# Performance work log

Hardware: AMD Instinct MI355X
Metric: run time of the kernel (lower is better)

Reference implementation:

```python
import jax, jax.numpy as jnp
import numpy as np

NUM_CENTERS = 256
CAPACITY = 2048
FEAT_DIM = 768
BATCH = 65536


def setup_inputs() -> dict:
    key = jax.random.key(0)
    k_bank, k_cid, k_idx = jax.random.split(key, 3)
    bank = jax.random.normal(k_bank, (NUM_CENTERS, CAPACITY, FEAT_DIM), dtype=jnp.float32)
    target_center_ids = jax.random.randint(k_cid, (BATCH,), 0, NUM_CENTERS, dtype=jnp.int64)
    rand_idx = jax.random.randint(k_idx, (BATCH,), 0, CAPACITY, dtype=jnp.int64)
    return {"bank": bank, "target_center_ids": target_center_ids, "rand_idx": rand_idx}


def reference(bank, target_center_ids, rand_idx):
    # get_counterfactual_noise(strategy='random') with a full bank:
    # per-sample gather bank[c_i, r_i] -> [B, feat_dim]
    return bank[target_center_ids, rand_idx]
```

## Files before the change

### kernel.cpp

```cpp
#include <hip/hip_runtime.h>

#define NUM_CENTERS 256
#define CAPACITY    2048
#define FEAT_DIM    768
#define BATCH       65536
#define VEC_PER_ROW (FEAT_DIM / 4)

#define THREADS 256
#define BLOCKS  2048

typedef float f32x4 __attribute__((ext_vector_type(4)));

__global__ __launch_bounds__(THREADS, 8) void gather_rows_kernel(
        const f32x4* __restrict__ bank,
        const int*   __restrict__ center_ids,
        const int*   __restrict__ rand_idx,
        f32x4*       __restrict__ out) {
    const int lane   = threadIdx.x & 63;
    const int wave   = (blockIdx.x << 2) | (threadIdx.x >> 6);
    const int nwaves = BLOCKS * (THREADS / 64);

#pragma unroll 2
    for (int s = wave; s < BATCH; s += nwaves) {
        const int c = __builtin_amdgcn_readfirstlane(center_ids[s]);
        const int r = __builtin_amdgcn_readfirstlane(rand_idx[s]);

        const f32x4* __restrict__ src =
            bank + ((long long)c * CAPACITY + (long long)r) * (long long)VEC_PER_ROW;
        f32x4* __restrict__ dst = out + (long long)s * (long long)VEC_PER_ROW;

        const f32x4 a = src[lane];
        const f32x4 b = src[lane + 64];
        const f32x4 d = src[lane + 128];
        __builtin_nontemporal_store(a, &dst[lane]);
        __builtin_nontemporal_store(b, &dst[lane + 64]);
        __builtin_nontemporal_store(d, &dst[lane + 128]);
    }
}

extern "C" void kernel_launch(void* const* d_in, const int* in_sizes, int n_in,
                              void* d_out, int out_size, void* d_ws, size_t ws_size,
                              hipStream_t stream) {
    const f32x4* bank       = (const f32x4*)d_in[0];
    const int*   center_ids = (const int*)d_in[1];
    const int*   rand_idx   = (const int*)d_in[2];
    f32x4*       out        = (f32x4*)d_out;

    gather_rows_kernel<<<BLOCKS, THREADS, 0, stream>>>(bank, center_ids, rand_idx, out);
}
```

Measured before the change: 1.816 ms.

## Launch one block per gathered row instead of grid-stride waves

```diff
diff --git a/kernel.cpp b/kernel.cpp
--- a/kernel.cpp
+++ b/kernel.cpp
@@ -6,36 +6,22 @@
 #define BATCH       65536
 #define VEC_PER_ROW (FEAT_DIM / 4)
 
-#define THREADS 256
-#define BLOCKS  2048
-
 typedef float f32x4 __attribute__((ext_vector_type(4)));
 
-__global__ __launch_bounds__(THREADS, 8) void gather_rows_kernel(
+__global__ __launch_bounds__(VEC_PER_ROW) void gather_rows_kernel(
         const f32x4* __restrict__ bank,
         const int*   __restrict__ center_ids,
         const int*   __restrict__ rand_idx,
         f32x4*       __restrict__ out) {
-    const int lane   = threadIdx.x & 63;
-    const int wave   = (blockIdx.x << 2) | (threadIdx.x >> 6);
-    const int nwaves = BLOCKS * (THREADS / 64);
+    const int s = blockIdx.x;
+    const int c = center_ids[s];
+    const int r = rand_idx[s];
 
-#pragma unroll 2
-    for (int s = wave; s < BATCH; s += nwaves) {
-        const int c = __builtin_amdgcn_readfirstlane(center_ids[s]);
-        const int r = __builtin_amdgcn_readfirstlane(rand_idx[s]);
+    const long long src_off = ((long long)c * CAPACITY + r) * (long long)VEC_PER_ROW;
+    const long long dst_off = (long long)s * (long long)VEC_PER_ROW;
 
-        const f32x4* __restrict__ src =
-            bank + ((long long)c * CAPACITY + (long long)r) * (long long)VEC_PER_ROW;
-        f32x4* __restrict__ dst = out + (long long)s * (long long)VEC_PER_ROW;
-
-        const f32x4 a = src[lane];
-        const f32x4 b = src[lane + 64];
-        const f32x4 d = src[lane + 128];
-        __builtin_nontemporal_store(a, &dst[lane]);
-        __builtin_nontemporal_store(b, &dst[lane + 64]);
-        __builtin_nontemporal_store(d, &dst[lane + 128]);
-    }
+    const f32x4 v = __builtin_nontemporal_load(&bank[src_off + threadIdx.x]);
+    __builtin_nontemporal_store(v, &out[dst_off + threadIdx.x]);
 }
 
 extern "C" void kernel_launch(void* const* d_in, const int* in_sizes, int n_in,
@@ -46,5 +32,5 @@
     const int*   rand_idx   = (const int*)d_in[2];
     f32x4*       out        = (f32x4*)d_out;
 
-    gather_rows_kernel<<<BLOCKS, THREADS, 0, stream>>>(bank, center_ids, rand_idx, out);
+    gather_rows_kernel<<<BATCH, VEC_PER_ROW, 0, stream>>>(bank, center_ids, rand_idx, out);
 }
```

Measured after the change: 1.832 ms. Within noise of the previous version (+0.9%).
